# Kernel optimization log

Measured on AMD Instinct MI355X. Metric: run time of the kernel, lower is better.

Reference implementation:

```python
import jax, jax.numpy as jnp
import numpy as np

N_NODES = 100000
N_EDGES = 1600000
IN_DIM, HID_DIM, OUT_DIM = 128, 64, 32


def gcn_conv(x, edge_index, W, b, n_nodes):
    """PyG GCNConv: add self-loops, symmetric deg^-1/2 normalization,
    linear transform, gather->scatter-sum aggregation, then bias."""
    loops = jnp.arange(n_nodes, dtype=edge_index.dtype)
    src = jnp.concatenate([edge_index[0], loops])  # [E+N]
    dst = jnp.concatenate([edge_index[1], loops])  # [E+N]
    # degree over targets (includes self-loops)
    deg = jax.ops.segment_sum(jnp.ones_like(dst, dtype=x.dtype), dst,
                              num_segments=n_nodes)
    dinv = jnp.where(deg > 0, jax.lax.rsqrt(deg), 0.0)
    norm = dinv[src] * dinv[dst]                   # [E+N]
    h = x @ W                                      # [N, F_out]
    msg = h[src] * norm[:, None]                   # gather + scale
    out = jax.ops.segment_sum(msg, dst, num_segments=n_nodes)
    return out + b


def setup_inputs() -> dict:
    key = jax.random.key(0)
    k1, k2, k3, k4 = jax.random.split(key, 4)
    x = jax.random.normal(k1, (N_NODES, IN_DIM), dtype=jnp.float32)
    edge_index = jax.random.randint(k2, (2, N_EDGES), 0, N_NODES,
                                    dtype=jnp.int64)
    # Glorot-ish init for weights, zero bias (PyG default: glorot + zeros)
    W1 = jax.random.normal(k3, (IN_DIM, HID_DIM), dtype=jnp.float32) * (1.0 / np.sqrt(IN_DIM))
    b1 = jnp.zeros((HID_DIM,), dtype=jnp.float32)
    W2 = jax.random.normal(k4, (HID_DIM, OUT_DIM), dtype=jnp.float32) * (1.0 / np.sqrt(HID_DIM))
    b2 = jnp.zeros((OUT_DIM,), dtype=jnp.float32)
    return {"x": x, "edge_index": edge_index, "W1": W1, "b1": b1,
            "W2": W2, "b2": b2}


def reference(x, edge_index, W1, b1, W2, b2):
    n = x.shape[0]
    h = jax.nn.relu(gcn_conv(x, edge_index, W1, b1, n))
    return gcn_conv(h, edge_index, W2, b2, n)
```

## Files before the change

kernel.cpp:

```cpp
#include <hip/hip_runtime.h>


#define BLK 256
#define BLKC 1024
#define EPT 8
#define BSHIFT 10
#define NPB 1024
#define SLOTB 18432
#define NBMAX 128

typedef unsigned int uint_t;
typedef unsigned short ushort_t;
typedef __attribute__((ext_vector_type(2))) float v2f;
typedef __attribute__((ext_vector_type(8))) short bf16x8;
typedef __attribute__((ext_vector_type(4))) float f32x4;

__device__ __forceinline__ uint_t f2bf(float x) {
    union { float f; uint_t u; } un; un.f = x;
    uint_t u = un.u;
    return (u + 0x7fffu + ((u >> 16) & 1u)) >> 16;
}

__device__ __forceinline__ void pkadd(v2f& a0, v2f& a1, v2f& a2, v2f& a3, uint4 v) {
    v2f p;
    p.x = __uint_as_float(v.x << 16); p.y = __uint_as_float(v.x & 0xffff0000u); a0 += p;
    p.x = __uint_as_float(v.y << 16); p.y = __uint_as_float(v.y & 0xffff0000u); a1 += p;
    p.x = __uint_as_float(v.z << 16); p.y = __uint_as_float(v.z & 0xffff0000u); a2 += p;
    p.x = __uint_as_float(v.w << 16); p.y = __uint_as_float(v.w & 0xffff0000u); a3 += p;
}

__device__ __forceinline__ bool detect64(const int* __restrict__ idx) {
    int z = 0;
#pragma unroll
    for (int i = 1; i < 32; i += 2) z |= idx[i];
    return z == 0;
}

__global__ void k_part(const int* __restrict__ idx, int* __restrict__ bcursor,
                       int* __restrict__ edge_part, int E, int nbuck) {
    __shared__ int h[NBMAX];
    __shared__ int rb[NBMAX];
    bool is64 = detect64(idx);
    int t = threadIdx.x, blk = blockIdx.x;
    for (int i = t; i < nbuck; i += BLK) h[i] = 0;
    __syncthreads();
    int base = blk * (BLK * EPT) + t;
    int dst[EPT], src[EPT];
#pragma unroll
    for (int k = 0; k < EPT; ++k) {
        int e = base + k * BLK;
        if (e < E) {
            dst[k] = is64 ? idx[2 * (E + e)] : idx[E + e];
            src[k] = is64 ? idx[2 * e] : idx[e];
            atomicAdd(&h[dst[k] >> BSHIFT], 1);
        } else {
            dst[k] = -1;
        }
    }
    __syncthreads();
    for (int i = t; i < nbuck; i += BLK) {
        int c = h[i];
        rb[i] = c ? atomicAdd(&bcursor[i], c) : 0;
        h[i] = 0;
    }
    __syncthreads();
#pragma unroll
    for (int k = 0; k < EPT; ++k) {
        if (dst[k] >= 0) {
            int b = dst[k] >> BSHIFT;
            int r = atomicAdd(&h[b], 1);
            edge_part[(size_t)b * SLOTB + rb[b] + r] =
                src[k] | ((dst[k] & (NPB - 1)) << 17);
        }
    }
}

__global__ __launch_bounds__(BLKC) void k_csr(
        const int* __restrict__ edge_part, const int* __restrict__ bcursor,
        int* __restrict__ row_ptr, int* __restrict__ deg, float* __restrict__ dinv,
        int* __restrict__ csr_src, int N, int nbuck) {
    __shared__ int cnt[NPB];
    __shared__ int off[NPB];
    int b = blockIdx.x, t = threadIdx.x;
    int node0 = b << BSHIFT;
    int nn = min(NPB, N - node0);
    int m = bcursor[b];
    size_t ebase = (size_t)b * SLOTB;
    cnt[t] = 0;
    __syncthreads();
    for (int e = t; e < m; e += BLKC)
        atomicAdd(&cnt[((unsigned)edge_part[ebase + e]) >> 17], 1);
    __syncthreads();
    off[t] = cnt[t];
    __syncthreads();
    for (int st = 1; st < BLKC; st <<= 1) {
        int v = (t >= st) ? off[t - st] : 0;
        __syncthreads();
        off[t] += v;
        __syncthreads();
    }
    int excl = off[t] - cnt[t];
    off[t] = excl;
    if (t < nn) {
        row_ptr[node0 + t] = (int)(ebase + excl);
        deg[node0 + t] = cnt[t];
        dinv[node0 + t] = rsqrtf((float)(cnt[t] + 1));
    }
    __syncthreads();
    for (int e = t; e < m; e += BLKC) {
        int p = edge_part[ebase + e];
        int dlo = ((unsigned)p) >> 17;
        int r = atomicAdd(&off[dlo], 1);
        csr_src[ebase + r] = p & 0x1FFFF;
    }
}

__global__ __launch_bounds__(256) void k_gemm1(
        const float* __restrict__ x, const float* __restrict__ W1,
        const float* __restrict__ dinv, ushort_t* __restrict__ hs1, int N) {
    __shared__ ushort_t xb[64][136];
    __shared__ ushort_t wb[64][136];
    int t = threadIdx.x;
    int rbase = blockIdx.x * 64;
    for (int i = t; i < 2048; i += BLK) {
        int k = i >> 4, n4 = i & 15;
        float4 w = ((const float4*)W1)[i];
        wb[4 * n4 + 0][k] = (ushort_t)f2bf(w.x);
        wb[4 * n4 + 1][k] = (ushort_t)f2bf(w.y);
        wb[4 * n4 + 2][k] = (ushort_t)f2bf(w.z);
        wb[4 * n4 + 3][k] = (ushort_t)f2bf(w.w);
    }
    for (int i = t; i < 2048; i += BLK) {
        int r = i >> 5, c4 = i & 31;
        int rr = rbase + r; if (rr >= N) rr = N - 1;
        float4 v = ((const float4*)x)[(size_t)rr * 32 + c4];
        uint2 p;
        p.x = f2bf(v.x) | (f2bf(v.y) << 16);
        p.y = f2bf(v.z) | (f2bf(v.w) << 16);
        *(uint2*)&xb[r][4 * c4] = p;
    }
    __syncthreads();
    int w = t >> 6, l = t & 63;
    int lane16 = l & 15, quad = l >> 4;
    int mrow = 16 * w + lane16;
    f32x4 acc0 = {0.f, 0.f, 0.f, 0.f}, acc1 = {0.f, 0.f, 0.f, 0.f};
    f32x4 acc2 = {0.f, 0.f, 0.f, 0.f}, acc3 = {0.f, 0.f, 0.f, 0.f};
#pragma unroll
    for (int kk = 0; kk < 4; ++kk) {
        int k0 = kk * 32 + quad * 8;
        bf16x8 a  = *(const bf16x8*)&xb[mrow][k0];
        bf16x8 b0 = *(const bf16x8*)&wb[lane16][k0];
        bf16x8 b1 = *(const bf16x8*)&wb[lane16 + 16][k0];
        bf16x8 b2 = *(const bf16x8*)&wb[lane16 + 32][k0];
        bf16x8 b3 = *(const bf16x8*)&wb[lane16 + 48][k0];
        acc0 = __builtin_amdgcn_mfma_f32_16x16x32_bf16(a, b0, acc0, 0, 0, 0);
        acc1 = __builtin_amdgcn_mfma_f32_16x16x32_bf16(a, b1, acc1, 0, 0, 0);
        acc2 = __builtin_amdgcn_mfma_f32_16x16x32_bf16(a, b2, acc2, 0, 0, 0);
        acc3 = __builtin_amdgcn_mfma_f32_16x16x32_bf16(a, b3, acc3, 0, 0, 0);
    }
    __syncthreads();
    int orow = 16 * w + quad * 4;
    float d0 = dinv[min(rbase + orow + 0, N - 1)];
    float d1 = dinv[min(rbase + orow + 1, N - 1)];
    float d2 = dinv[min(rbase + orow + 2, N - 1)];
    float d3 = dinv[min(rbase + orow + 3, N - 1)];
    xb[orow + 0][lane16]      = (ushort_t)f2bf(acc0.x * d0);
    xb[orow + 1][lane16]      = (ushort_t)f2bf(acc0.y * d1);
    xb[orow + 2][lane16]      = (ushort_t)f2bf(acc0.z * d2);
    xb[orow + 3][lane16]      = (ushort_t)f2bf(acc0.w * d3);
    xb[orow + 0][lane16 + 16] = (ushort_t)f2bf(acc1.x * d0);
    xb[orow + 1][lane16 + 16] = (ushort_t)f2bf(acc1.y * d1);
    xb[orow + 2][lane16 + 16] = (ushort_t)f2bf(acc1.z * d2);
    xb[orow + 3][lane16 + 16] = (ushort_t)f2bf(acc1.w * d3);
    xb[orow + 0][lane16 + 32] = (ushort_t)f2bf(acc2.x * d0);
    xb[orow + 1][lane16 + 32] = (ushort_t)f2bf(acc2.y * d1);
    xb[orow + 2][lane16 + 32] = (ushort_t)f2bf(acc2.z * d2);
    xb[orow + 3][lane16 + 32] = (ushort_t)f2bf(acc2.w * d3);
    xb[orow + 0][lane16 + 48] = (ushort_t)f2bf(acc3.x * d0);
    xb[orow + 1][lane16 + 48] = (ushort_t)f2bf(acc3.y * d1);
    xb[orow + 2][lane16 + 48] = (ushort_t)f2bf(acc3.z * d2);
    xb[orow + 3][lane16 + 48] = (ushort_t)f2bf(acc3.w * d3);
    __syncthreads();
    for (int i = t; i < 512; i += BLK) {
        int r = i >> 3, c8 = i & 7;
        int rr = rbase + r;
        if (rr < N) {
            uint4 v = *(const uint4*)&xb[r][8 * c8];
            *(uint4*)&hs1[(size_t)rr * 64 + 8 * c8] = v;
        }
    }
}

__global__ void k_agg1(const uint_t* __restrict__ hs1, const int* __restrict__ row_ptr,
                       const int* __restrict__ deg, const int* __restrict__ csr_src,
                       const float* __restrict__ dinv, const float* __restrict__ b1,
                       ushort_t* __restrict__ a1b, int N) {
    int node = (blockIdx.x * blockDim.x + threadIdx.x) >> 6;
    if (node >= N) return;
    int lane = threadIdx.x & 63;
    int g = lane >> 3;
    int c = lane & 7;
    const uint4* H = (const uint4*)hs1;
    v2f a0 = {0.f, 0.f}, a1_ = {0.f, 0.f}, a2 = {0.f, 0.f}, a3 = {0.f, 0.f};
    float dn = dinv[node];
    int beg = row_ptr[node], tot = deg[node];
    int jal = (lane < tot) ? csr_src[beg + lane] : 0;
    if (g == 0) pkadd(a0, a1_, a2, a3, H[(size_t)node * 8 + c]);
    int nt = (tot + 7) >> 3;
    int t = 0;
    for (; t + 1 < nt; t += 2) {
        int s0 = g + 8 * t, s1 = s0 + 8;
        int j0 = __shfl(jal, s0 & 63, 64);
        int j1 = __shfl(jal, s1 & 63, 64);
        if (s0 >= 64) j0 = csr_src[beg + s0];
        bool p1 = s1 < tot;
        if (s1 >= 64 && p1) j1 = csr_src[beg + s1];
        uint4 v0 = H[(size_t)j0 * 8 + c];
        uint4 v1;
        if (p1) v1 = H[(size_t)j1 * 8 + c];
        pkadd(a0, a1_, a2, a3, v0);
        if (p1) pkadd(a0, a1_, a2, a3, v1);
    }
    for (; t < nt; ++t) {
        int s = g + 8 * t;
        int j = __shfl(jal, s & 63, 64);
        bool p = s < tot;
        if (s >= 64 && p) j = csr_src[beg + s];
        if (p) pkadd(a0, a1_, a2, a3, H[(size_t)j * 8 + c]);
    }
#pragma unroll
    for (int m = 8; m <= 32; m <<= 1) {
        a0.x += __shfl_xor(a0.x, m, 64); a0.y += __shfl_xor(a0.y, m, 64);
        a1_.x += __shfl_xor(a1_.x, m, 64); a1_.y += __shfl_xor(a1_.y, m, 64);
        a2.x += __shfl_xor(a2.x, m, 64); a2.y += __shfl_xor(a2.y, m, 64);
        a3.x += __shfl_xor(a3.x, m, 64); a3.y += __shfl_xor(a3.y, m, 64);
    }
    if (g == 0) {
        const float4* B = (const float4*)b1;
        float4 bv0 = B[2 * c], bv1 = B[2 * c + 1];
        float o0 = fmaxf(fmaf(a0.x, dn, bv0.x), 0.f);
        float o1 = fmaxf(fmaf(a0.y, dn, bv0.y), 0.f);
        float o2 = fmaxf(fmaf(a1_.x, dn, bv0.z), 0.f);
        float o3 = fmaxf(fmaf(a1_.y, dn, bv0.w), 0.f);
        float o4 = fmaxf(fmaf(a2.x, dn, bv1.x), 0.f);
        float o5 = fmaxf(fmaf(a2.y, dn, bv1.y), 0.f);
        float o6 = fmaxf(fmaf(a3.x, dn, bv1.z), 0.f);
        float o7 = fmaxf(fmaf(a3.y, dn, bv1.w), 0.f);
        uint4 o;
        o.x = f2bf(o0) | (f2bf(o1) << 16);
        o.y = f2bf(o2) | (f2bf(o3) << 16);
        o.z = f2bf(o4) | (f2bf(o5) << 16);
        o.w = f2bf(o6) | (f2bf(o7) << 16);
        ((uint4*)a1b)[(size_t)node * 8 + c] = o;
    }
}

__global__ __launch_bounds__(256) void k_gemm2(
        const ushort_t* __restrict__ a1b, const float* __restrict__ W2,
        const float* __restrict__ dinv, ushort_t* __restrict__ hs2, int N) {
    __shared__ ushort_t ab[64][72];
    __shared__ ushort_t wb[32][72];
    int t = threadIdx.x;
    int rbase = blockIdx.x * 64;
    for (int i = t; i < 512; i += BLK) {
        int k = i >> 3, n4 = i & 7;
        float4 w = ((const float4*)W2)[i];
        wb[4 * n4 + 0][k] = (ushort_t)f2bf(w.x);
        wb[4 * n4 + 1][k] = (ushort_t)f2bf(w.y);
        wb[4 * n4 + 2][k] = (ushort_t)f2bf(w.z);
        wb[4 * n4 + 3][k] = (ushort_t)f2bf(w.w);
    }
    for (int i = t; i < 512; i += BLK) {
        int r = i >> 3, c8 = i & 7;
        int rr = rbase + r; if (rr >= N) rr = N - 1;
        uint4 v = ((const uint4*)a1b)[(size_t)rr * 8 + c8];
        *(uint4*)&ab[r][8 * c8] = v;
    }
    __syncthreads();
    int w = t >> 6, l = t & 63;
    int lane16 = l & 15, quad = l >> 4;
    int mrow = 16 * w + lane16;
    f32x4 acc0 = {0.f, 0.f, 0.f, 0.f}, acc1 = {0.f, 0.f, 0.f, 0.f};
#pragma unroll
    for (int kk = 0; kk < 2; ++kk) {
        int k0 = kk * 32 + quad * 8;
        bf16x8 a  = *(const bf16x8*)&ab[mrow][k0];
        bf16x8 b0 = *(const bf16x8*)&wb[lane16][k0];
        bf16x8 b1 = *(const bf16x8*)&wb[lane16 + 16][k0];
        acc0 = __builtin_amdgcn_mfma_f32_16x16x32_bf16(a, b0, acc0, 0, 0, 0);
        acc1 = __builtin_amdgcn_mfma_f32_16x16x32_bf16(a, b1, acc1, 0, 0, 0);
    }
    __syncthreads();
    int orow = 16 * w + quad * 4;
    float d0 = dinv[min(rbase + orow + 0, N - 1)];
    float d1 = dinv[min(rbase + orow + 1, N - 1)];
    float d2 = dinv[min(rbase + orow + 2, N - 1)];
    float d3 = dinv[min(rbase + orow + 3, N - 1)];
    ab[orow + 0][lane16]      = (ushort_t)f2bf(acc0.x * d0);
    ab[orow + 1][lane16]      = (ushort_t)f2bf(acc0.y * d1);
    ab[orow + 2][lane16]      = (ushort_t)f2bf(acc0.z * d2);
    ab[orow + 3][lane16]      = (ushort_t)f2bf(acc0.w * d3);
    ab[orow + 0][lane16 + 16] = (ushort_t)f2bf(acc1.x * d0);
    ab[orow + 1][lane16 + 16] = (ushort_t)f2bf(acc1.y * d1);
    ab[orow + 2][lane16 + 16] = (ushort_t)f2bf(acc1.z * d2);
    ab[orow + 3][lane16 + 16] = (ushort_t)f2bf(acc1.w * d3);
    __syncthreads();
    for (int i = t; i < 256; i += BLK) {
        int r = i >> 2, c4 = i & 3;
        int rr = rbase + r;
        if (rr < N) {
            uint4 v = *(const uint4*)&ab[r][8 * c4];
            *(uint4*)&hs2[(size_t)rr * 32 + 8 * c4] = v;
        }
    }
}

__global__ void k_agg2(const uint_t* __restrict__ hs2, const int* __restrict__ row_ptr,
                       const int* __restrict__ deg, const int* __restrict__ csr_src,
                       const float* __restrict__ dinv, const float* __restrict__ b2,
                       float* __restrict__ out, int N) {
    int node = (blockIdx.x * blockDim.x + threadIdx.x) >> 6;
    if (node >= N) return;
    int lane = threadIdx.x & 63;
    int g = lane >> 2;
    int c = lane & 3;
    const uint4* H = (const uint4*)hs2;
    v2f a0 = {0.f, 0.f}, a1_ = {0.f, 0.f}, a2 = {0.f, 0.f}, a3 = {0.f, 0.f};
    int beg = row_ptr[node], tot = deg[node];
    int jal = (lane < tot) ? csr_src[beg + lane] : 0;
    if (g == 0) pkadd(a0, a1_, a2, a3, H[(size_t)node * 4 + c]);
    int nt = (tot + 15) >> 4;
    int t = 0;
    for (; t + 1 < nt; t += 2) {
        int s0 = g + 16 * t, s1 = s0 + 16;
        int j0 = __shfl(jal, s0 & 63, 64);
        int j1 = __shfl(jal, s1 & 63, 64);
        if (s0 >= 64) j0 = csr_src[beg + s0];
        bool p1 = s1 < tot;
        if (s1 >= 64 && p1) j1 = csr_src[beg + s1];
        uint4 v0 = H[(size_t)j0 * 4 + c];
        uint4 v1;
        if (p1) v1 = H[(size_t)j1 * 4 + c];
        pkadd(a0, a1_, a2, a3, v0);
        if (p1) pkadd(a0, a1_, a2, a3, v1);
    }
    for (; t < nt; ++t) {
        int s = g + 16 * t;
        int j = __shfl(jal, s & 63, 64);
        bool p = s < tot;
        if (s >= 64 && p) j = csr_src[beg + s];
        if (p) pkadd(a0, a1_, a2, a3, H[(size_t)j * 4 + c]);
    }
#pragma unroll
    for (int m = 4; m <= 32; m <<= 1) {
        a0.x += __shfl_xor(a0.x, m, 64); a0.y += __shfl_xor(a0.y, m, 64);
        a1_.x += __shfl_xor(a1_.x, m, 64); a1_.y += __shfl_xor(a1_.y, m, 64);
        a2.x += __shfl_xor(a2.x, m, 64); a2.y += __shfl_xor(a2.y, m, 64);
        a3.x += __shfl_xor(a3.x, m, 64); a3.y += __shfl_xor(a3.y, m, 64);
    }
    if (g == 0) {
        float s = dinv[node];
        const float4* B = (const float4*)b2;
        float4 bv0 = B[2 * c], bv1 = B[2 * c + 1];
        float4 o0, o1;
        o0.x = fmaf(a0.x, s, bv0.x);
        o0.y = fmaf(a0.y, s, bv0.y);
        o0.z = fmaf(a1_.x, s, bv0.z);
        o0.w = fmaf(a1_.y, s, bv0.w);
        o1.x = fmaf(a2.x, s, bv1.x);
        o1.y = fmaf(a2.y, s, bv1.y);
        o1.z = fmaf(a3.x, s, bv1.z);
        o1.w = fmaf(a3.y, s, bv1.w);
        float4* O = (float4*)out;
        O[(size_t)node * 8 + 2 * c] = o0;
        O[(size_t)node * 8 + 2 * c + 1] = o1;
    }
}

extern "C" void kernel_launch(void* const* d_in, const int* in_sizes, int n_in,
                              void* d_out, int out_size, void* d_ws, size_t ws_size,
                              hipStream_t stream) {
    const float* x  = (const float*)d_in[0];
    const int*   idx = (const int*)d_in[1];
    const float* W1 = (const float*)d_in[2];
    const float* b1 = (const float*)d_in[3];
    const float* W2 = (const float*)d_in[4];
    const float* b2 = (const float*)d_in[5];
    float* out = (float*)d_out;

    const int N = in_sizes[0] / 128;
    const int E = in_sizes[1] / 2;
    const int nbuck = (N + NPB - 1) >> BSHIFT;
    const int PB = (E + BLK * EPT - 1) / (BLK * EPT);

    char* ws = (char*)d_ws;
    size_t off = 0;
    auto alloc = [&](size_t bytes) -> char* {
        char* p = ws + off;
        off = (off + bytes + 255) & ~(size_t)255;
        return p;
    };
    float* dinv     = (float*)alloc((size_t)N * 4);
    int*   row_ptr  = (int*)alloc((size_t)N * 4);
    int*   deg      = (int*)alloc((size_t)N * 4);
    int*   bcursor  = (int*)alloc((size_t)nbuck * 4);
    int*   csr_src  = (int*)alloc((size_t)nbuck * SLOTB * 4);
    size_t ep_bytes = (size_t)nbuck * SLOTB * 4;
    size_t h1_bytes = (size_t)N * 64 * 2;
    int*   edge_part = (int*)alloc(ep_bytes > h1_bytes ? ep_bytes : h1_bytes);
    ushort_t* a1b   = (ushort_t*)alloc((size_t)N * 64 * 2);
    ushort_t* hs1   = (ushort_t*)edge_part;
    ushort_t* hs2   = hs1;

    hipMemsetAsync(bcursor, 0, (size_t)nbuck * 4, stream);
    k_part<<<PB, BLK, 0, stream>>>(idx, bcursor, edge_part, E, nbuck);
    k_csr<<<nbuck, BLKC, 0, stream>>>(edge_part, bcursor, row_ptr, deg, dinv,
                                      csr_src, N, nbuck);
    k_gemm1<<<(N + 63) / 64, BLK, 0, stream>>>(x, W1, dinv, hs1, N);
    k_agg1<<<(N + 3) / 4, BLK, 0, stream>>>((const uint_t*)hs1, row_ptr, deg,
                                            csr_src, dinv, b1, a1b, N);
    k_gemm2<<<(N + 63) / 64, BLK, 0, stream>>>(a1b, W2, dinv, hs2, N);
    k_agg2<<<(N + 3) / 4, BLK, 0, stream>>>((const uint_t*)hs2, row_ptr, deg,
                                            csr_src, dinv, b2, out, N);
}
```

Measured before the change: 250.3 us.

## Assign multiple nodes per wavefront in aggregation kernels, removing cross-lane reductions

Both aggregation kernels now map one node to each 8-lane (layer 1) or 4-lane (layer 2) group instead of one node per 64-lane wave. Each group loads its neighbour indices in small chunks and broadcasts them with shuffles, so the shuffle-xor reduction tree and the mostly idle output lanes go away. The grids shrink accordingly. In exchange, a wave runs as long as its highest-degree node, so uneven degrees leave some lanes idle.

```diff
diff --git a/kernel.cpp b/kernel.cpp
--- a/kernel.cpp
+++ b/kernel.cpp
@@ -195,47 +195,30 @@
                        const int* __restrict__ deg, const int* __restrict__ csr_src,
                        const float* __restrict__ dinv, const float* __restrict__ b1,
                        ushort_t* __restrict__ a1b, int N) {
-    int node = (blockIdx.x * blockDim.x + threadIdx.x) >> 6;
-    if (node >= N) return;
     int lane = threadIdx.x & 63;
     int g = lane >> 3;
     int c = lane & 7;
+    int wavebase = ((blockIdx.x * blockDim.x + threadIdx.x) >> 6) * 8;
+    int node = wavebase + g;
+    bool alive = node < N;
+    int nodeC = alive ? node : N - 1;
     const uint4* H = (const uint4*)hs1;
     v2f a0 = {0.f, 0.f}, a1_ = {0.f, 0.f}, a2 = {0.f, 0.f}, a3 = {0.f, 0.f};
-    float dn = dinv[node];
-    int beg = row_ptr[node], tot = deg[node];
-    int jal = (lane < tot) ? csr_src[beg + lane] : 0;
-    if (g == 0) pkadd(a0, a1_, a2, a3, H[(size_t)node * 8 + c]);
-    int nt = (tot + 7) >> 3;
-    int t = 0;
-    for (; t + 1 < nt; t += 2) {
-        int s0 = g + 8 * t, s1 = s0 + 8;
-        int j0 = __shfl(jal, s0 & 63, 64);
-        int j1 = __shfl(jal, s1 & 63, 64);
-        if (s0 >= 64) j0 = csr_src[beg + s0];
-        bool p1 = s1 < tot;
-        if (s1 >= 64 && p1) j1 = csr_src[beg + s1];
-        uint4 v0 = H[(size_t)j0 * 8 + c];
-        uint4 v1;
-        if (p1) v1 = H[(size_t)j1 * 8 + c];
-        pkadd(a0, a1_, a2, a3, v0);
-        if (p1) pkadd(a0, a1_, a2, a3, v1);
-    }
-    for (; t < nt; ++t) {
-        int s = g + 8 * t;
-        int j = __shfl(jal, s & 63, 64);
-        bool p = s < tot;
-        if (s >= 64 && p) j = csr_src[beg + s];
-        if (p) pkadd(a0, a1_, a2, a3, H[(size_t)j * 8 + c]);
-    }
-#pragma unroll
-    for (int m = 8; m <= 32; m <<= 1) {
-        a0.x += __shfl_xor(a0.x, m, 64); a0.y += __shfl_xor(a0.y, m, 64);
-        a1_.x += __shfl_xor(a1_.x, m, 64); a1_.y += __shfl_xor(a1_.y, m, 64);
-        a2.x += __shfl_xor(a2.x, m, 64); a2.y += __shfl_xor(a2.y, m, 64);
-        a3.x += __shfl_xor(a3.x, m, 64); a3.y += __shfl_xor(a3.y, m, 64);
-    }
-    if (g == 0) {
+    float dn = dinv[nodeC];
+    int beg = row_ptr[nodeC];
+    int tot = alive ? deg[nodeC] : 0;
+    pkadd(a0, a1_, a2, a3, H[(size_t)nodeC * 8 + c]);
+    int gbase = lane & 0x38;
+    for (int eb = 0; __any(eb < tot); eb += 8) {
+        int jal = 0;
+        if (eb + c < tot) jal = csr_src[beg + eb + c];
+#pragma unroll
+        for (int e = 0; e < 8; ++e) {
+            int j = __shfl(jal, gbase + e, 64);
+            if (eb + e < tot) pkadd(a0, a1_, a2, a3, H[(size_t)j * 8 + c]);
+        }
+    }
+    if (alive) {
         const float4* B = (const float4*)b1;
         float4 bv0 = B[2 * c], bv1 = B[2 * c + 1];
         float o0 = fmaxf(fmaf(a0.x, dn, bv0.x), 0.f);
@@ -319,58 +302,41 @@
                        const int* __restrict__ deg, const int* __restrict__ csr_src,
                        const float* __restrict__ dinv, const float* __restrict__ b2,
                        float* __restrict__ out, int N) {
-    int node = (blockIdx.x * blockDim.x + threadIdx.x) >> 6;
-    if (node >= N) return;
     int lane = threadIdx.x & 63;
     int g = lane >> 2;
     int c = lane & 3;
+    int wavebase = ((blockIdx.x * blockDim.x + threadIdx.x) >> 6) * 16;
+    int node = wavebase + g;
+    bool alive = node < N;
+    int nodeC = alive ? node : N - 1;
     const uint4* H = (const uint4*)hs2;
     v2f a0 = {0.f, 0.f}, a1_ = {0.f, 0.f}, a2 = {0.f, 0.f}, a3 = {0.f, 0.f};
-    int beg = row_ptr[node], tot = deg[node];
-    int jal = (lane < tot) ? csr_src[beg + lane] : 0;
-    if (g == 0) pkadd(a0, a1_, a2, a3, H[(size_t)node * 4 + c]);
-    int nt = (tot + 15) >> 4;
-    int t = 0;
-    for (; t + 1 < nt; t += 2) {
-        int s0 = g + 16 * t, s1 = s0 + 16;
-        int j0 = __shfl(jal, s0 & 63, 64);
-        int j1 = __shfl(jal, s1 & 63, 64);
-        if (s0 >= 64) j0 = csr_src[beg + s0];
-        bool p1 = s1 < tot;
-        if (s1 >= 64 && p1) j1 = csr_src[beg + s1];
-        uint4 v0 = H[(size_t)j0 * 4 + c];
-        uint4 v1;
-        if (p1) v1 = H[(size_t)j1 * 4 + c];
-        pkadd(a0, a1_, a2, a3, v0);
-        if (p1) pkadd(a0, a1_, a2, a3, v1);
-    }
-    for (; t < nt; ++t) {
-        int s = g + 16 * t;
-        int j = __shfl(jal, s & 63, 64);
-        bool p = s < tot;
-        if (s >= 64 && p) j = csr_src[beg + s];
-        if (p) pkadd(a0, a1_, a2, a3, H[(size_t)j * 4 + c]);
-    }
-#pragma unroll
-    for (int m = 4; m <= 32; m <<= 1) {
-        a0.x += __shfl_xor(a0.x, m, 64); a0.y += __shfl_xor(a0.y, m, 64);
-        a1_.x += __shfl_xor(a1_.x, m, 64); a1_.y += __shfl_xor(a1_.y, m, 64);
-        a2.x += __shfl_xor(a2.x, m, 64); a2.y += __shfl_xor(a2.y, m, 64);
-        a3.x += __shfl_xor(a3.x, m, 64); a3.y += __shfl_xor(a3.y, m, 64);
-    }
-    if (g == 0) {
-        float s = dinv[node];
+    float dn = dinv[nodeC];
+    int beg = row_ptr[nodeC];
+    int tot = alive ? deg[nodeC] : 0;
+    pkadd(a0, a1_, a2, a3, H[(size_t)nodeC * 4 + c]);
+    int gbase = lane & 0x3C;
+    for (int eb = 0; __any(eb < tot); eb += 4) {
+        int jal = 0;
+        if (eb + c < tot) jal = csr_src[beg + eb + c];
+#pragma unroll
+        for (int e = 0; e < 4; ++e) {
+            int j = __shfl(jal, gbase + e, 64);
+            if (eb + e < tot) pkadd(a0, a1_, a2, a3, H[(size_t)j * 4 + c]);
+        }
+    }
+    if (alive) {
         const float4* B = (const float4*)b2;
         float4 bv0 = B[2 * c], bv1 = B[2 * c + 1];
         float4 o0, o1;
-        o0.x = fmaf(a0.x, s, bv0.x);
-        o0.y = fmaf(a0.y, s, bv0.y);
-        o0.z = fmaf(a1_.x, s, bv0.z);
-        o0.w = fmaf(a1_.y, s, bv0.w);
-        o1.x = fmaf(a2.x, s, bv1.x);
-        o1.y = fmaf(a2.y, s, bv1.y);
-        o1.z = fmaf(a3.x, s, bv1.z);
-        o1.w = fmaf(a3.y, s, bv1.w);
+        o0.x = fmaf(a0.x, dn, bv0.x);
+        o0.y = fmaf(a0.y, dn, bv0.y);
+        o0.z = fmaf(a1_.x, dn, bv0.z);
+        o0.w = fmaf(a1_.y, dn, bv0.w);
+        o1.x = fmaf(a2.x, dn, bv1.x);
+        o1.y = fmaf(a2.y, dn, bv1.y);
+        o1.z = fmaf(a3.x, dn, bv1.z);
+        o1.w = fmaf(a3.y, dn, bv1.w);
         float4* O = (float4*)out;
         O[(size_t)node * 8 + 2 * c] = o0;
         O[(size_t)node * 8 + 2 * c + 1] = o1;
@@ -417,9 +383,9 @@
     k_csr<<<nbuck, BLKC, 0, stream>>>(edge_part, bcursor, row_ptr, deg, dinv,
                                       csr_src, N, nbuck);
     k_gemm1<<<(N + 63) / 64, BLK, 0, stream>>>(x, W1, dinv, hs1, N);
-    k_agg1<<<(N + 3) / 4, BLK, 0, stream>>>((const uint_t*)hs1, row_ptr, deg,
-                                            csr_src, dinv, b1, a1b, N);
+    k_agg1<<<(N * 8 + BLK - 1) / BLK / 4 * 4 + 4, BLK, 0, stream>>>(
+        (const uint_t*)hs1, row_ptr, deg, csr_src, dinv, b1, a1b, N);
     k_gemm2<<<(N + 63) / 64, BLK, 0, stream>>>(a1b, W2, dinv, hs2, N);
-    k_agg2<<<(N + 3) / 4, BLK, 0, stream>>>((const uint_t*)hs2, row_ptr, deg,
-                                            csr_src, dinv, b2, out, N);
-}
+    k_agg2<<<(N * 4 + BLK - 1) / BLK, BLK, 0, stream>>>(
+        (const uint_t*)hs2, row_ptr, deg, csr_src, dinv, b2, out, N);
+}
```

Measured after the change: 229.7 us. -8.2%, faster.
